# Kernel tuning notes

Hardware: AMD Instinct MI355X
Metric: run time of the kernel (lower is better)

The kernel has to match this reference:

```python
import jax, jax.numpy as jnp
import numpy as np
from jax import lax

B, IC, OC, K, INF = 16, 64, 1, 3, 64
HID = IC * OC * K * K          # 576
PER_GROUP = HID // INF         # 9 outputs per group in grouped 1x1 conv
H = W = 256
DN = ('NCHW', 'OIHW', 'NCHW')


def setup_inputs() -> dict:
    key = jax.random.key(0)
    ks = jax.random.split(key, 9)
    s = 0.02
    return {
        'x1': jax.random.normal(ks[0], (B, IC, H, W), jnp.float32),
        'weight': jax.random.normal(ks[1], (B, INF, H, W), jnp.float32),
        'ca_fc1_w': jax.random.normal(ks[2], (INF // 8, INF), jnp.float32) * s,
        'ca_fc2_w': jax.random.normal(ks[3], (INF, INF // 8), jnp.float32) * s,
        'sa_w': jax.random.normal(ks[4], (1, 2, 7, 7), jnp.float32) * s,
        'pk_conv1_w': jax.random.normal(ks[5], (INF, INF), jnp.float32) * s,
        'pk_conv1_b': jax.random.normal(ks[6], (INF,), jnp.float32) * s,
        'pk_conv2_w': jax.random.normal(ks[7], (HID,), jnp.float32) * s,  # groups=INF, in/group=1, 1x1
        'pk_conv2_b': jax.random.normal(ks[8], (HID,), jnp.float32) * s,
    }


def reference(x1, weight, ca_fc1_w, ca_fc2_w, sa_w, pk_conv1_w, pk_conv1_b, pk_conv2_w, pk_conv2_b):
    b, in_planes, h, w = x1.shape
    # ---- ChannelAttention: shared MLP on global avg & max pooled features ----
    avg = jnp.mean(weight, axis=(2, 3))              # [B, INF]
    mx = jnp.max(weight, axis=(2, 3))                # [B, INF]
    mlp = lambda v: jax.nn.relu(v @ ca_fc1_w.T) @ ca_fc2_w.T
    ca = jax.nn.sigmoid(mlp(avg) + mlp(mx))[:, :, None, None]  # [B, INF, 1, 1]
    wg = ca * weight
    # ---- SpatialAttention: channel mean/max -> 7x7 conv -> sigmoid ----
    sp_in = jnp.concatenate([jnp.mean(wg, axis=1, keepdims=True),
                             jnp.max(wg, axis=1, keepdims=True)], axis=1)  # [B,2,H,W]
    sa = jax.nn.sigmoid(lax.conv_general_dilated(
        sp_in, sa_w, (1, 1), ((3, 3), (3, 3)), dimension_numbers=DN))      # [B,1,H,W]
    wg = sa * wg
    # ---- Kernel generator: 1x1 conv (+bias) -> global avg pool -> grouped 1x1 conv ----
    c1 = jnp.einsum('bchw,oc->bohw', wg, pk_conv1_w) + pk_conv1_b[None, :, None, None]
    pooled = jnp.mean(c1, axis=(2, 3))                # [B, INF]
    # grouped conv (groups=INF, in/group=1): out o depends only on channel o//PER_GROUP
    kern = jnp.repeat(pooled, PER_GROUP, axis=1) * pk_conv2_w[None, :] + pk_conv2_b[None, :]  # [B, HID]
    kernel = kern.reshape(b * OC, IC, K, K)
    # ---- dynamic per-sample conv: groups = batch ----
    pad = (K - 1) // 2
    out = lax.conv_general_dilated(
        x1.reshape(1, b * in_planes, h, w), kernel, (1, 1), ((pad, pad), (pad, pad)),
        dimension_numbers=DN, feature_group_count=b)
    return out.reshape(b, OC, h, w)
```

## Files before the change

### kernel.cpp

```cpp
#include <hip/hip_runtime.h>
#include <math.h>

#define B_ 16
#define C_ 64
#define H_ 256
#define W_ 256
#define HW_ 65536

typedef __attribute__((ext_vector_type(4))) float f4v;
typedef __attribute__((ext_vector_type(2))) float f2v;
typedef __attribute__((ext_vector_type(2))) unsigned int u2v;

__device__ __forceinline__ float waveSum(float v) {
#pragma unroll
    for (int o = 32; o > 0; o >>= 1) v += __shfl_down(v, o, 64);
    return v;
}
__device__ __forceinline__ float waveMax(float v) {
#pragma unroll
    for (int o = 32; o > 0; o >>= 1) v = fmaxf(v, __shfl_down(v, o, 64));
    return v;
}

__global__ __launch_bounds__(512) void reduce_weight_q(const float* __restrict__ w,
                              u2v* __restrict__ wq,
                              float* __restrict__ wsum, float* __restrict__ wmax) {
    int bc = blockIdx.x;
    const f4v* p = (const f4v*)(w + (size_t)bc * HW_);
    u2v* q = wq + (size_t)bc * (HW_ / 8);
    float s = 0.f, m = -INFINITY;
#pragma unroll 4
    for (int i = threadIdx.x; i < HW_ / 8; i += 512) {
        f4v a = __builtin_nontemporal_load(p + 2 * i);
        f4v c = __builtin_nontemporal_load(p + 2 * i + 1);
        s += (a.x + a.y) + (a.z + a.w) + (c.x + c.y) + (c.z + c.w);
        m = fmaxf(m, fmaxf(fmaxf(a.x, a.y), fmaxf(a.z, a.w)));
        m = fmaxf(m, fmaxf(fmaxf(c.x, c.y), fmaxf(c.z, c.w)));
        unsigned int lo = __builtin_amdgcn_cvt_pk_fp8_f32(a.x, a.y, 0u, false);
        lo = __builtin_amdgcn_cvt_pk_fp8_f32(a.z, a.w, lo, true);
        unsigned int hi = __builtin_amdgcn_cvt_pk_fp8_f32(c.x, c.y, 0u, false);
        hi = __builtin_amdgcn_cvt_pk_fp8_f32(c.z, c.w, hi, true);
        u2v o; o.x = lo; o.y = hi;
        q[i] = o;
    }
    __shared__ float ts[8], tm[8];
    int wid = threadIdx.x >> 6, lane = threadIdx.x & 63;
    s = waveSum(s);
    m = waveMax(m);
    if (lane == 0) { ts[wid] = s; tm[wid] = m; }
    __syncthreads();
    if (threadIdx.x == 0) {
        float a = 0.f, qm = -INFINITY;
#pragma unroll
        for (int j = 0; j < 8; ++j) { a += ts[j]; qm = fmaxf(qm, tm[j]); }
        wsum[bc] = a;
        wmax[bc] = qm;
    }
}

__global__ __launch_bounds__(256) void ca_spatial(const u2v* __restrict__ wq,
                           const float* __restrict__ wsum, const float* __restrict__ wmax,
                           const float* __restrict__ fc1, const float* __restrict__ fc2,
                           float* __restrict__ spm, float* __restrict__ spx,
                           float* __restrict__ ca_out) {
    int b = blockIdx.y;
    int t = threadIdx.x;
    __shared__ float hid[16];
    __shared__ float cas[64];
    if (t < 16) {
        int j = t & 7;
        const float* src = (t < 8) ? wsum : wmax;
        float scale = (t < 8) ? (1.f / (float)HW_) : 1.f;
        float s = 0.f;
#pragma unroll 8
        for (int c = 0; c < 64; ++c) s += fc1[j * 64 + c] * (src[b * 64 + c] * scale);
        hid[t] = fmaxf(s, 0.f);
    }
    __syncthreads();
    if (t < 64) {
        float o = 0.f;
#pragma unroll
        for (int j = 0; j < 8; ++j) o += (hid[j] + hid[8 + j]) * fc2[t * 8 + j];
        float c = 1.f / (1.f + expf(-o));
        cas[t] = c;
        if (blockIdx.x == 0) ca_out[b * 64 + t] = c;
    }
    __syncthreads();

    int pix8 = blockIdx.x * 256 + t;
    const u2v* base = wq + (size_t)b * 64 * (HW_ / 8);
    float s[8], mm[8];
#pragma unroll
    for (int j = 0; j < 8; ++j) { s[j] = 0.f; mm[j] = -INFINITY; }
#pragma unroll 8
    for (int c = 0; c < 64; ++c) {
        u2v u = base[(size_t)c * (HW_ / 8) + pix8];
        float a = cas[c];
        f2v p01 = __builtin_amdgcn_cvt_pk_f32_fp8(u.x, false);
        f2v p23 = __builtin_amdgcn_cvt_pk_f32_fp8(u.x, true);
        f2v p45 = __builtin_amdgcn_cvt_pk_f32_fp8(u.y, false);
        f2v p67 = __builtin_amdgcn_cvt_pk_f32_fp8(u.y, true);
        float v0 = a * p01.x, v1 = a * p01.y, v2 = a * p23.x, v3 = a * p23.y;
        float v4 = a * p45.x, v5 = a * p45.y, v6 = a * p67.x, v7 = a * p67.y;
        s[0] += v0; s[1] += v1; s[2] += v2; s[3] += v3;
        s[4] += v4; s[5] += v5; s[6] += v6; s[7] += v7;
        mm[0] = fmaxf(mm[0], v0); mm[1] = fmaxf(mm[1], v1);
        mm[2] = fmaxf(mm[2], v2); mm[3] = fmaxf(mm[3], v3);
        mm[4] = fmaxf(mm[4], v4); mm[5] = fmaxf(mm[5], v5);
        mm[6] = fmaxf(mm[6], v6); mm[7] = fmaxf(mm[7], v7);
    }
    const float inv = 1.f / 64.f;
    float4* pm = (float4*)spm + (size_t)b * (HW_ / 4) + pix8 * 2;
    float4* px = (float4*)spx + (size_t)b * (HW_ / 4) + pix8 * 2;
    pm[0] = make_float4(s[0] * inv, s[1] * inv, s[2] * inv, s[3] * inv);
    pm[1] = make_float4(s[4] * inv, s[5] * inv, s[6] * inv, s[7] * inv);
    px[0] = make_float4(mm[0], mm[1], mm[2], mm[3]);
    px[1] = make_float4(mm[4], mm[5], mm[6], mm[7]);
}

__global__ void sa_conv(const float* __restrict__ spm, const float* __restrict__ spx,
                        const float* __restrict__ sw, float* __restrict__ sa) {
    int b = blockIdx.y, y = blockIdx.x, x = threadIdx.x;
    const float* in0 = spm + (size_t)b * HW_;
    const float* in1 = spx + (size_t)b * HW_;
    float acc = 0.f;
#pragma unroll
    for (int ky = 0; ky < 7; ++ky) {
        int yy = y + ky - 3;
        if (yy < 0 || yy >= H_) continue;
        const float* r0 = in0 + yy * W_;
        const float* r1 = in1 + yy * W_;
#pragma unroll
        for (int kx = 0; kx < 7; ++kx) {
            int xx = x + kx - 3;
            if (xx < 0 || xx >= W_) continue;
            acc += r0[xx] * sw[ky * 7 + kx] + r1[xx] * sw[49 + ky * 7 + kx];
        }
    }
    sa[(size_t)b * HW_ + y * W_ + x] = 1.f / (1.f + expf(-acc));
}

__global__ __launch_bounds__(512) void weighted_reduce(const u2v* __restrict__ wq,
                                const float* __restrict__ sa,
                                float* __restrict__ sval) {
    int d = blockIdx.x;
    int bc = ((d & 7) << 7) + (d >> 3);
    int b = bc >> 6;
    const u2v* wp = wq + (size_t)bc * (HW_ / 8);
    const float4* sp = (const float4*)(sa + (size_t)b * HW_);
    float s = 0.f;
#pragma unroll 4
    for (int i = threadIdx.x; i < HW_ / 8; i += 512) {
        u2v u = wp[i];
        float4 q0 = sp[2 * i], q1 = sp[2 * i + 1];
        f2v p01 = __builtin_amdgcn_cvt_pk_f32_fp8(u.x, false);
        f2v p23 = __builtin_amdgcn_cvt_pk_f32_fp8(u.x, true);
        f2v p45 = __builtin_amdgcn_cvt_pk_f32_fp8(u.y, false);
        f2v p67 = __builtin_amdgcn_cvt_pk_f32_fp8(u.y, true);
        s += p01.x * q0.x + p01.y * q0.y + p23.x * q0.z + p23.y * q0.w
           + p45.x * q1.x + p45.y * q1.y + p67.x * q1.z + p67.y * q1.w;
    }
    __shared__ float ts[8];
    int wid = threadIdx.x >> 6, lane = threadIdx.x & 63;
    s = waveSum(s);
    if (lane == 0) ts[wid] = s;
    __syncthreads();
    if (threadIdx.x == 0) {
        float a = 0.f;
#pragma unroll
        for (int j = 0; j < 8; ++j) a += ts[j];
        sval[bc] = a * (1.f / (float)HW_);
    }
}

__global__ __launch_bounds__(256) void final_conv(const float* __restrict__ x1,
                           const float* __restrict__ ca, const float* __restrict__ sval,
                           const float* __restrict__ pk1w, const float* __restrict__ pk1b,
                           const float* __restrict__ pk2w, const float* __restrict__ pk2b,
                           float* __restrict__ out) {
    int d = blockIdx.x;
    int gid = ((d & 7) << 7) + (d >> 3);
    int b = gid >> 6;
    int y0 = (gid & 63) * 4;
    int t = threadIdx.x;
    __shared__ float wg[64];
    __shared__ float kern[64][9];
    if (t < 64) wg[t] = ca[b * 64 + t] * sval[b * 64 + t];
    __syncthreads();
    if (t < 64) {
        float p = pk1b[t];
#pragma unroll 8
        for (int c = 0; c < 64; ++c) p += pk1w[t * 64 + c] * wg[c];
#pragma unroll
        for (int j = 0; j < 9; ++j) kern[t][j] = p * pk2w[t * 9 + j] + pk2b[t * 9 + j];
    }
    __syncthreads();

    int x = t;
    float acc[4] = {0.f, 0.f, 0.f, 0.f};

    for (int ic = 0; ic < 64; ++ic) {
        const float* plane = x1 + ((size_t)(b * 64 + ic) << 16);
        float k0 = kern[ic][0], k1 = kern[ic][1], k2 = kern[ic][2];
        float k3 = kern[ic][3], k4 = kern[ic][4], k5 = kern[ic][5];
        float k6 = kern[ic][6], k7 = kern[ic][7], k8 = kern[ic][8];
#pragma unroll
        for (int j = -1; j <= 4; ++j) {
            int yy = y0 + j;
            float m = 0.f, z = 0.f, p = 0.f;
            if (yy >= 0 && yy < H_) {
                const float* row = plane + yy * W_;
                z = row[x];
                m = (x > 0) ? row[x - 1] : 0.f;
                p = (x < W_ - 1) ? row[x + 1] : 0.f;
            }
            if (j <= 2) acc[j + 1] += m * k0 + z * k1 + p * k2;
            if (j >= 0 && j <= 3) acc[j] += m * k3 + z * k4 + p * k5;
            if (j >= 1) acc[j - 1] += m * k6 + z * k7 + p * k8;
        }
    }
#pragma unroll
    for (int r = 0; r < 4; ++r)
        out[(size_t)b * HW_ + (size_t)(y0 + r) * W_ + x] = acc[r];
}

extern "C" void kernel_launch(void* const* d_in, const int* in_sizes, int n_in,
                              void* d_out, int out_size, void* d_ws, size_t ws_size,
                              hipStream_t stream) {
    const float* x1     = (const float*)d_in[0];
    const float* weight = (const float*)d_in[1];
    const float* fc1    = (const float*)d_in[2];
    const float* fc2    = (const float*)d_in[3];
    const float* saw    = (const float*)d_in[4];
    const float* pk1w   = (const float*)d_in[5];
    const float* pk1b   = (const float*)d_in[6];
    const float* pk2w   = (const float*)d_in[7];
    const float* pk2b   = (const float*)d_in[8];
    float* out = (float*)d_out;

    float* ws   = (float*)d_ws;
    float* wsum = ws;
    float* wmax = ws + 1024;
    float* ca   = ws + 2048;
    float* sval = ws + 3072;
    float* spm  = ws + 16384;
    float* spx  = spm + (size_t)B_ * HW_;
    float* sa   = spx + (size_t)B_ * HW_;
    u2v*   wq   = (u2v*)(ws + 16384 + 3u * 1048576u);

    reduce_weight_q<<<dim3(B_ * C_), 512, 0, stream>>>(weight, wq, wsum, wmax);
    ca_spatial<<<dim3(32, B_), 256, 0, stream>>>(wq, wsum, wmax, fc1, fc2, spm, spx, ca);
    sa_conv<<<dim3(H_, B_), 256, 0, stream>>>(spm, spx, saw, sa);
    weighted_reduce<<<dim3(B_ * C_), 512, 0, stream>>>(wq, sa, sval);
    final_conv<<<dim3(B_ * C_), 256, 0, stream>>>(x1, ca, sval, pk1w, pk1b, pk2w, pk2b, out);
}
```

Before: 201.4 us.

## Fuse all five stages into one cooperative persistent kernel with grid syncs

Replaces the five separate launches with a single cooperative kernel of 512 blocks of 256 threads. Grid-wide syncs separate the stages: weight reduction with FP8 quantisation, channel attention plus spatial mean/max, the 7x7 spatial conv, the weighted reduce, and the final dynamic conv. Each block handles two units per stage, and the later stages use a swizzled block index. The aim is to remove launch gaps and tail effects between kernels, at the cost of less parallelism per stage and the overhead of grid syncs. If the cooperative launch fails, the code falls back to the original five-kernel path.

```diff
diff --git a/kernel.cpp b/kernel.cpp
--- a/kernel.cpp
+++ b/kernel.cpp
@@ -1,5 +1,8 @@
 #include <hip/hip_runtime.h>
+#include <hip/hip_cooperative_groups.h>
 #include <math.h>
+
+namespace cg = cooperative_groups;
 
 #define B_ 16
 #define C_ 64
@@ -20,6 +23,225 @@
 #pragma unroll
     for (int o = 32; o > 0; o >>= 1) v = fmaxf(v, __shfl_down(v, o, 64));
     return v;
+}
+
+__global__ __launch_bounds__(256, 4) void fused_all(
+    const float* __restrict__ x1, const float* __restrict__ w,
+    const float* __restrict__ fc1, const float* __restrict__ fc2,
+    const float* __restrict__ sw,
+    const float* __restrict__ pk1w, const float* __restrict__ pk1b,
+    const float* __restrict__ pk2w, const float* __restrict__ pk2b,
+    float* __restrict__ out,
+    float* __restrict__ wsum, float* __restrict__ wmax,
+    float* __restrict__ sval, float* __restrict__ spm,
+    float* __restrict__ spx, float* __restrict__ sa,
+    u2v* __restrict__ wq)
+{
+    cg::grid_group grid = cg::this_grid();
+    const int bx = blockIdx.x;
+    const int t = threadIdx.x;
+    const int wid = t >> 6, lane = t & 63;
+
+    __shared__ float ts[4], tm[4];
+    __shared__ float hid[16];
+    __shared__ float cas[64];
+    __shared__ float kern[64][9];
+
+#pragma unroll
+    for (int it = 0; it < 2; ++it) {
+        const int bc = bx + it * 512;
+        const f4v* p = (const f4v*)(w + (size_t)bc * HW_);
+        u2v* q = wq + (size_t)bc * (HW_ / 8);
+        float s = 0.f, m = -INFINITY;
+#pragma unroll 4
+        for (int i = t; i < HW_ / 8; i += 256) {
+            f4v a = __builtin_nontemporal_load(p + 2 * i);
+            f4v c = __builtin_nontemporal_load(p + 2 * i + 1);
+            s += (a.x + a.y) + (a.z + a.w) + (c.x + c.y) + (c.z + c.w);
+            m = fmaxf(m, fmaxf(fmaxf(a.x, a.y), fmaxf(a.z, a.w)));
+            m = fmaxf(m, fmaxf(fmaxf(c.x, c.y), fmaxf(c.z, c.w)));
+            unsigned int lo = __builtin_amdgcn_cvt_pk_fp8_f32(a.x, a.y, 0u, false);
+            lo = __builtin_amdgcn_cvt_pk_fp8_f32(a.z, a.w, lo, true);
+            unsigned int hi = __builtin_amdgcn_cvt_pk_fp8_f32(c.x, c.y, 0u, false);
+            hi = __builtin_amdgcn_cvt_pk_fp8_f32(c.z, c.w, hi, true);
+            u2v o; o.x = lo; o.y = hi;
+            q[i] = o;
+        }
+        s = waveSum(s);
+        m = waveMax(m);
+        if (lane == 0) { ts[wid] = s; tm[wid] = m; }
+        __syncthreads();
+        if (t == 0) {
+            wsum[bc] = ts[0] + ts[1] + ts[2] + ts[3];
+            wmax[bc] = fmaxf(fmaxf(tm[0], tm[1]), fmaxf(tm[2], tm[3]));
+        }
+        __syncthreads();
+    }
+    grid.sync();
+
+    {
+        const int b = bx >> 5;
+        if (t < 16) {
+            int j = t & 7;
+            const float* src = (t < 8) ? wsum : wmax;
+            float scale = (t < 8) ? (1.f / (float)HW_) : 1.f;
+            float s = 0.f;
+#pragma unroll 8
+            for (int c = 0; c < 64; ++c) s += fc1[j * 64 + c] * (src[b * 64 + c] * scale);
+            hid[t] = fmaxf(s, 0.f);
+        }
+        __syncthreads();
+        if (t < 64) {
+            float o = 0.f;
+#pragma unroll
+            for (int j = 0; j < 8; ++j) o += (hid[j] + hid[8 + j]) * fc2[t * 8 + j];
+            cas[t] = 1.f / (1.f + expf(-o));
+        }
+        __syncthreads();
+
+        const int pix8 = (bx & 31) * 256 + t;
+        const u2v* base = wq + (size_t)b * 64 * (HW_ / 8);
+        float s[8], mm[8];
+#pragma unroll
+        for (int j = 0; j < 8; ++j) { s[j] = 0.f; mm[j] = -INFINITY; }
+#pragma unroll 8
+        for (int c = 0; c < 64; ++c) {
+            u2v u = base[(size_t)c * (HW_ / 8) + pix8];
+            float a = cas[c];
+            f2v p01 = __builtin_amdgcn_cvt_pk_f32_fp8(u.x, false);
+            f2v p23 = __builtin_amdgcn_cvt_pk_f32_fp8(u.x, true);
+            f2v p45 = __builtin_amdgcn_cvt_pk_f32_fp8(u.y, false);
+            f2v p67 = __builtin_amdgcn_cvt_pk_f32_fp8(u.y, true);
+            float v0 = a * p01.x, v1 = a * p01.y, v2 = a * p23.x, v3 = a * p23.y;
+            float v4 = a * p45.x, v5 = a * p45.y, v6 = a * p67.x, v7 = a * p67.y;
+            s[0] += v0; s[1] += v1; s[2] += v2; s[3] += v3;
+            s[4] += v4; s[5] += v5; s[6] += v6; s[7] += v7;
+            mm[0] = fmaxf(mm[0], v0); mm[1] = fmaxf(mm[1], v1);
+            mm[2] = fmaxf(mm[2], v2); mm[3] = fmaxf(mm[3], v3);
+            mm[4] = fmaxf(mm[4], v4); mm[5] = fmaxf(mm[5], v5);
+            mm[6] = fmaxf(mm[6], v6); mm[7] = fmaxf(mm[7], v7);
+        }
+        const float inv = 1.f / 64.f;
+        float4* pm = (float4*)spm + (size_t)b * (HW_ / 4) + pix8 * 2;
+        float4* px = (float4*)spx + (size_t)b * (HW_ / 4) + pix8 * 2;
+        pm[0] = make_float4(s[0] * inv, s[1] * inv, s[2] * inv, s[3] * inv);
+        pm[1] = make_float4(s[4] * inv, s[5] * inv, s[6] * inv, s[7] * inv);
+        px[0] = make_float4(mm[0], mm[1], mm[2], mm[3]);
+        px[1] = make_float4(mm[4], mm[5], mm[6], mm[7]);
+    }
+    grid.sync();
+
+#pragma unroll
+    for (int r = 0; r < 8; ++r) {
+        const int yg = bx * 8 + r;
+        const int b = yg >> 8, y = yg & 255, x = t;
+        const float* in0 = spm + (size_t)b * HW_;
+        const float* in1 = spx + (size_t)b * HW_;
+        float acc = 0.f;
+#pragma unroll
+        for (int ky = 0; ky < 7; ++ky) {
+            int yy = y + ky - 3;
+            if (yy < 0 || yy >= H_) continue;
+            const float* r0 = in0 + yy * W_;
+            const float* r1 = in1 + yy * W_;
+#pragma unroll
+            for (int kx = 0; kx < 7; ++kx) {
+                int xx = x + kx - 3;
+                if (xx < 0 || xx >= W_) continue;
+                acc += r0[xx] * sw[ky * 7 + kx] + r1[xx] * sw[49 + ky * 7 + kx];
+            }
+        }
+        sa[(size_t)b * HW_ + y * W_ + x] = 1.f / (1.f + expf(-acc));
+    }
+    grid.sync();
+
+#pragma unroll
+    for (int it = 0; it < 2; ++it) {
+        const int v = bx + it * 512;
+        const int bc = ((v & 7) << 7) + (v >> 3);
+        const int b = bc >> 6;
+        const u2v* wp = wq + (size_t)bc * (HW_ / 8);
+        const float4* sp = (const float4*)(sa + (size_t)b * HW_);
+        float s = 0.f;
+#pragma unroll 4
+        for (int i = t; i < HW_ / 8; i += 256) {
+            u2v u = wp[i];
+            float4 q0 = sp[2 * i], q1 = sp[2 * i + 1];
+            f2v p01 = __builtin_amdgcn_cvt_pk_f32_fp8(u.x, false);
+            f2v p23 = __builtin_amdgcn_cvt_pk_f32_fp8(u.x, true);
+            f2v p45 = __builtin_amdgcn_cvt_pk_f32_fp8(u.y, false);
+            f2v p67 = __builtin_amdgcn_cvt_pk_f32_fp8(u.y, true);
+            s += p01.x * q0.x + p01.y * q0.y + p23.x * q0.z + p23.y * q0.w
+               + p45.x * q1.x + p45.y * q1.y + p67.x * q1.z + p67.y * q1.w;
+        }
+        s = waveSum(s);
+        if (lane == 0) ts[wid] = s;
+        __syncthreads();
+        if (t == 0) sval[bc] = ts[0] + ts[1] + ts[2] + ts[3];
+        __syncthreads();
+    }
+    grid.sync();
+
+#pragma unroll
+    for (int it = 0; it < 2; ++it) {
+        const int v = bx + it * 512;
+        const int gid = ((v & 7) << 7) + (v >> 3);
+        const int b = gid >> 6;
+        const int y0 = (gid & 63) * 4;
+        if (t < 16) {
+            int j = t & 7;
+            const float* src = (t < 8) ? wsum : wmax;
+            float scale = (t < 8) ? (1.f / (float)HW_) : 1.f;
+            float s = 0.f;
+#pragma unroll 8
+            for (int c = 0; c < 64; ++c) s += fc1[j * 64 + c] * (src[b * 64 + c] * scale);
+            hid[t] = fmaxf(s, 0.f);
+        }
+        __syncthreads();
+        if (t < 64) {
+            float o = 0.f;
+#pragma unroll
+            for (int j = 0; j < 8; ++j) o += (hid[j] + hid[8 + j]) * fc2[t * 8 + j];
+            float ca = 1.f / (1.f + expf(-o));
+            cas[t] = ca * (sval[b * 64 + t] * (1.f / (float)HW_));
+        }
+        __syncthreads();
+        if (t < 64) {
+            float p = pk1b[t];
+#pragma unroll 8
+            for (int c = 0; c < 64; ++c) p += pk1w[t * 64 + c] * cas[c];
+#pragma unroll
+            for (int j = 0; j < 9; ++j) kern[t][j] = p * pk2w[t * 9 + j] + pk2b[t * 9 + j];
+        }
+        __syncthreads();
+
+        const int x = t;
+        float acc[4] = {0.f, 0.f, 0.f, 0.f};
+        for (int ic = 0; ic < 64; ++ic) {
+            const float* plane = x1 + ((size_t)(b * 64 + ic) << 16);
+            float k0 = kern[ic][0], k1 = kern[ic][1], k2 = kern[ic][2];
+            float k3 = kern[ic][3], k4 = kern[ic][4], k5 = kern[ic][5];
+            float k6 = kern[ic][6], k7 = kern[ic][7], k8 = kern[ic][8];
+#pragma unroll
+            for (int j = -1; j <= 4; ++j) {
+                int yy = y0 + j;
+                float m = 0.f, z = 0.f, p = 0.f;
+                if (yy >= 0 && yy < H_) {
+                    const float* row = plane + yy * W_;
+                    z = row[x];
+                    m = (x > 0) ? row[x - 1] : 0.f;
+                    p = (x < W_ - 1) ? row[x + 1] : 0.f;
+                }
+                if (j <= 2) acc[j + 1] += m * k0 + z * k1 + p * k2;
+                if (j >= 0 && j <= 3) acc[j] += m * k3 + z * k4 + p * k5;
+                if (j >= 1) acc[j - 1] += m * k6 + z * k7 + p * k8;
+            }
+        }
+#pragma unroll
+        for (int r = 0; r < 4; ++r)
+            out[(size_t)b * HW_ + (size_t)(y0 + r) * W_ + x] = acc[r];
+        __syncthreads();
+    }
 }
 
 __global__ __launch_bounds__(512) void reduce_weight_q(const float* __restrict__ w,
@@ -198,7 +420,6 @@
 
     int x = t;
     float acc[4] = {0.f, 0.f, 0.f, 0.f};
-
     for (int ic = 0; ic < 64; ++ic) {
         const float* plane = x1 + ((size_t)(b * 64 + ic) << 16);
         float k0 = kern[ic][0], k1 = kern[ic][1], k2 = kern[ic][2];
@@ -248,9 +469,24 @@
     float* sa   = spx + (size_t)B_ * HW_;
     u2v*   wq   = (u2v*)(ws + 16384 + 3u * 1048576u);
 
-    reduce_weight_q<<<dim3(B_ * C_), 512, 0, stream>>>(weight, wq, wsum, wmax);
-    ca_spatial<<<dim3(32, B_), 256, 0, stream>>>(wq, wsum, wmax, fc1, fc2, spm, spx, ca);
-    sa_conv<<<dim3(H_, B_), 256, 0, stream>>>(spm, spx, saw, sa);
-    weighted_reduce<<<dim3(B_ * C_), 512, 0, stream>>>(wq, sa, sval);
-    final_conv<<<dim3(B_ * C_), 256, 0, stream>>>(x1, ca, sval, pk1w, pk1b, pk2w, pk2b, out);
-}
+    float* svalc = ws + 4096;
+
+    void* args[] = {
+        (void*)&x1, (void*)&weight, (void*)&fc1, (void*)&fc2, (void*)&saw,
+        (void*)&pk1w, (void*)&pk1b, (void*)&pk2w, (void*)&pk2b,
+        (void*)&out, (void*)&wsum, (void*)&wmax, (void*)&svalc,
+        (void*)&spm, (void*)&spx, (void*)&sa, (void*)&wq
+    };
+    hipError_t err = hipLaunchCooperativeKernel((const void*)fused_all, dim3(512),
+                                                dim3(256), args, 0, stream);
+    if (err != hipSuccess) {
+        (void)hipGetLastError();
+        reduce_weight_q<<<dim3(B_ * C_), 512, 0, stream>>>(weight, wq, wsum, wmax);
+        ca_spatial<<<dim3(32, B_), 256, 0, stream>>>(wq, wsum, wmax, fc1, fc2,
+                                                     spm, spx, ca);
+        sa_conv<<<dim3(H_, B_), 256, 0, stream>>>(spm, spx, saw, sa);
+        weighted_reduce<<<dim3(B_ * C_), 512, 0, stream>>>(wq, sa, sval);
+        final_conv<<<dim3(B_ * C_), 256, 0, stream>>>(x1, ca, sval,
+                                                      pk1w, pk1b, pk2w, pk2b, out);
+    }
+}
```

After: 506.9 us (median of 2 runs). 152% more time.

## Remap dynamic conv threads to float4 column tiles with interior fast path

Applied to the files above, without the earlier changes.

The per-sample 3x3 conv previously had each thread compute one column across four rows, reading scalar taps and reusing loaded rows vertically. Now each thread owns four adjacent columns of one row, loads a float4 plus two halo scalars per input row, and takes a branch-free path for interior rows. This aims to widen global loads and cut scalar load instructions. In exchange it gives up the vertical row reuse: each thread reads three rows per channel for one output row instead of six rows for four.

```diff
diff --git a/kernel.cpp b/kernel.cpp
--- a/kernel.cpp
+++ b/kernel.cpp
@@ -196,32 +196,58 @@
     }
     __syncthreads();
 
-    int x = t;
-    float acc[4] = {0.f, 0.f, 0.f, 0.f};
-
-    for (int ic = 0; ic < 64; ++ic) {
-        const float* plane = x1 + ((size_t)(b * 64 + ic) << 16);
-        float k0 = kern[ic][0], k1 = kern[ic][1], k2 = kern[ic][2];
-        float k3 = kern[ic][3], k4 = kern[ic][4], k5 = kern[ic][5];
-        float k6 = kern[ic][6], k7 = kern[ic][7], k8 = kern[ic][8];
-#pragma unroll
-        for (int j = -1; j <= 4; ++j) {
-            int yy = y0 + j;
-            float m = 0.f, z = 0.f, p = 0.f;
-            if (yy >= 0 && yy < H_) {
+    const int col4 = t & 63;
+    const int y = y0 + (t >> 6);
+    const int x0 = col4 * 4;
+    const bool interior = (y >= 1) && (y <= 254);
+    float4 acc = make_float4(0.f, 0.f, 0.f, 0.f);
+
+    if (interior) {
+        for (int ic = 0; ic < 64; ++ic) {
+            const float* plane = x1 + ((size_t)(b * 64 + ic) << 16);
+            const float4* p4 = (const float4*)plane;
+#pragma unroll
+            for (int j = 0; j < 3; ++j) {
+                const int yy = y + j - 1;
                 const float* row = plane + yy * W_;
-                z = row[x];
-                m = (x > 0) ? row[x - 1] : 0.f;
-                p = (x < W_ - 1) ? row[x + 1] : 0.f;
+                float4 v = p4[yy * (W_ / 4) + col4];
+                float lw = (col4 > 0) ? row[x0 - 1] : 0.f;
+                float rw = (col4 < 63) ? row[x0 + 4] : 0.f;
+                float ka = kern[ic][j * 3 + 0];
+                float kb = kern[ic][j * 3 + 1];
+                float kc = kern[ic][j * 3 + 2];
+                acc.x += lw  * ka + v.x * kb + v.y * kc;
+                acc.y += v.x * ka + v.y * kb + v.z * kc;
+                acc.z += v.y * ka + v.z * kb + v.w * kc;
+                acc.w += v.z * ka + v.w * kb + rw  * kc;
             }
-            if (j <= 2) acc[j + 1] += m * k0 + z * k1 + p * k2;
-            if (j >= 0 && j <= 3) acc[j] += m * k3 + z * k4 + p * k5;
-            if (j >= 1) acc[j - 1] += m * k6 + z * k7 + p * k8;
         }
-    }
-#pragma unroll
-    for (int r = 0; r < 4; ++r)
-        out[(size_t)b * HW_ + (size_t)(y0 + r) * W_ + x] = acc[r];
+    } else {
+        for (int ic = 0; ic < 64; ++ic) {
+            const float* plane = x1 + ((size_t)(b * 64 + ic) << 16);
+            const float4* p4 = (const float4*)plane;
+#pragma unroll
+            for (int j = 0; j < 3; ++j) {
+                const int yy = y + j - 1;
+                float4 v = make_float4(0.f, 0.f, 0.f, 0.f);
+                float lw = 0.f, rw = 0.f;
+                if (yy >= 0 && yy < H_) {
+                    const float* row = plane + yy * W_;
+                    v = p4[yy * (W_ / 4) + col4];
+                    lw = (col4 > 0) ? row[x0 - 1] : 0.f;
+                    rw = (col4 < 63) ? row[x0 + 4] : 0.f;
+                }
+                float ka = kern[ic][j * 3 + 0];
+                float kb = kern[ic][j * 3 + 1];
+                float kc = kern[ic][j * 3 + 2];
+                acc.x += lw  * ka + v.x * kb + v.y * kc;
+                acc.y += v.x * ka + v.y * kb + v.z * kc;
+                acc.z += v.y * ka + v.z * kb + v.w * kc;
+                acc.w += v.z * ka + v.w * kb + rw  * kc;
+            }
+        }
+    }
+    ((float4*)(out + (size_t)b * HW_ + (size_t)y * W_))[col4] = acc;
 }
 
 extern "C" void kernel_launch(void* const* d_in, const int* in_sizes, int n_in,
```

Result: slower. 260.4 us (+29.3%).
